# Performance work log

Measured on AMD Instinct MI355X. Metric: run time of the kernel, lower is better.

Reference implementation:

```python
import jax, jax.numpy as jnp
import numpy as np

N_EMBD = 768
N_HEAD = 12

def setup_inputs() -> dict:
    key = jax.random.key(0)
    k_x, k_wa, k_ba, k_wp, k_bp = jax.random.split(key, 5)
    C = N_EMBD
    scale = 1.0 / np.sqrt(C)
    return {
        "x": jax.random.normal(k_x, (2, 4096, C), dtype=jnp.float32),
        "W_attn": jax.random.normal(k_wa, (C, 3 * C), dtype=jnp.float32) * scale,
        "b_attn": jax.random.normal(k_ba, (3 * C,), dtype=jnp.float32) * 0.01,
        "W_proj": jax.random.normal(k_wp, (C, C), dtype=jnp.float32) * scale,
        "b_proj": jax.random.normal(k_bp, (C,), dtype=jnp.float32) * 0.01,
    }

def reference(x, W_attn, b_attn, W_proj, b_proj) -> jnp.ndarray:
    B, T, C = x.shape
    H = N_HEAD
    D = C // H  # head dim
    qkv = x @ W_attn + b_attn                     # [B,T,3C]
    q, k, v = jnp.split(qkv, 3, axis=-1)
    # [B,T,C] -> [B,H,T,D]
    q = q.reshape(B, T, H, D).transpose(0, 2, 1, 3)
    k = k.reshape(B, T, H, D).transpose(0, 2, 1, 3)
    v = v.reshape(B, T, H, D).transpose(0, 2, 1, 3)
    scores = jnp.einsum("bhqd,bhkd->bhqk", q, k) * (1.0 / jnp.sqrt(jnp.float32(D)))
    attn = jax.nn.softmax(scores, axis=-1)        # dropout p=0.0 -> identity
    y = jnp.einsum("bhqk,bhkd->bhqd", attn, v)    # [B,H,T,D]
    y = y.transpose(0, 2, 1, 3).reshape(B, T, C)
    return y @ W_proj + b_proj
```

## Files before the change

kernel.cpp:

```cpp
#include <hip/hip_runtime.h>
#include <stdint.h>

#define NB 2
#define NT 4096
#define NC 768
#define NH 12
#define ND 64
#define NBT (NB*NT)
#define NQKV (3*NC)

typedef _Float16 half_t;
typedef __attribute__((ext_vector_type(8))) _Float16 f16x8;
typedef __attribute__((ext_vector_type(4))) _Float16 f16x4;
typedef __attribute__((ext_vector_type(2))) __fp16 fp16x2;
typedef __attribute__((ext_vector_type(4))) float f32x4;

#define MFMA16(a,b,c) __builtin_amdgcn_mfma_f32_16x16x32_f16((a),(b),(c),0,0,0)

__device__ __forceinline__ void load_lds16(const void* g, void* l) {
    auto gp = reinterpret_cast<__attribute__((address_space(1))) char*>(reinterpret_cast<uintptr_t>(g));
    auto lp = reinterpret_cast<__attribute__((address_space(3))) char*>(reinterpret_cast<uintptr_t>(l));
    __builtin_amdgcn_global_load_lds(gp, lp, 16, 0, 0);
}

__global__ __launch_bounds__(256) void k_pack(const float* __restrict__ in, half_t* __restrict__ out, int n4) {
    int i = blockIdx.x * 256 + threadIdx.x;
    if (i >= n4) return;
    float4 f = reinterpret_cast<const float4*>(in)[i];
    f16x4 h;
    h[0] = (half_t)f.x; h[1] = (half_t)f.y; h[2] = (half_t)f.z; h[3] = (half_t)f.w;
    reinterpret_cast<f16x4*>(out)[i] = h;
}

__global__ __launch_bounds__(256) void k_packT(const float* __restrict__ in, half_t* __restrict__ out, int N, int K) {
    int idx = blockIdx.x * 256 + threadIdx.x;
    if (idx >= N * K) return;
    int n = idx / K, k = idx - n * K;
    out[idx] = (half_t)in[(size_t)k * N + n];
}

template<int OUTF32>
__global__ __launch_bounds__(256) void k_gemm(const half_t* __restrict__ A, const half_t* __restrict__ Bt,
                                              const float* __restrict__ bias, void* __restrict__ out, int N) {
    __shared__ half_t As[128 * 32];
    __shared__ half_t Bs[128 * 32];
    const int tid = threadIdx.x;
    const int lane = tid & 63, w = tid >> 6;
    const int m0 = blockIdx.x * 128, n0 = blockIdx.y * 128;
    const int wm = (w >> 1) * 64, wn = (w & 1) * 64;
    const int lr = lane & 15, lk = (lane >> 4) * 8;

    f32x4 acc[4][4];
#pragma unroll
    for (int a = 0; a < 4; ++a)
#pragma unroll
        for (int bq = 0; bq < 4; ++bq) acc[a][bq] = (f32x4){0.f, 0.f, 0.f, 0.f};

    const int c0 = tid, c1 = 256 + tid;
    const int ldsbase = (tid & ~63) * 16;

    for (int ks = 0; ks < 24; ++ks) {
        const int k0 = ks * 32;
        __syncthreads();
        load_lds16(A  + (size_t)(m0 + (c0 >> 2)) * NC + k0 + (c0 & 3) * 8, (char*)As + ldsbase);
        load_lds16(Bt + (size_t)(n0 + (c0 >> 2)) * NC + k0 + (c0 & 3) * 8, (char*)Bs + ldsbase);
        load_lds16(A  + (size_t)(m0 + (c1 >> 2)) * NC + k0 + (c1 & 3) * 8, (char*)As + 4096 + ldsbase);
        load_lds16(Bt + (size_t)(n0 + (c1 >> 2)) * NC + k0 + (c1 & 3) * 8, (char*)Bs + 4096 + ldsbase);
        __syncthreads();
        f16x8 af[4], bf[4];
#pragma unroll
        for (int mi = 0; mi < 4; ++mi)
            af[mi] = *reinterpret_cast<const f16x8*>(&As[(wm + mi * 16 + lr) * 32 + lk]);
#pragma unroll
        for (int ni = 0; ni < 4; ++ni)
            bf[ni] = *reinterpret_cast<const f16x8*>(&Bs[(wn + ni * 16 + lr) * 32 + lk]);
#pragma unroll
        for (int mi = 0; mi < 4; ++mi)
#pragma unroll
            for (int ni = 0; ni < 4; ++ni)
                acc[mi][ni] = MFMA16(af[mi], bf[ni], acc[mi][ni]);
    }

    const int rg = (lane >> 4) * 4;
#pragma unroll
    for (int ni = 0; ni < 4; ++ni) {
        const int gn = n0 + wn + ni * 16 + lr;
        const float bv = bias[gn];
#pragma unroll
        for (int mi = 0; mi < 4; ++mi)
#pragma unroll
            for (int i = 0; i < 4; ++i) {
                const size_t gm = (size_t)(m0 + wm + mi * 16 + rg + i);
                const float v = acc[mi][ni][i] + bv;
                if (OUTF32) reinterpret_cast<float*>(out)[gm * N + gn] = v;
                else        reinterpret_cast<half_t*>(out)[gm * N + gn] = (half_t)v;
            }
    }
}

__global__ __launch_bounds__(256) void k_vt(const half_t* __restrict__ qkv, half_t* __restrict__ Vt) {
    __shared__ half_t tile[64][72];
    const int tid = threadIdx.x;
    const int t0 = blockIdx.x * 64, bh = blockIdx.y;
    const int b = bh / NH, h = bh - b * NH;
    {
        const int tl = tid >> 2, dc = (tid & 3) * 16;
        const half_t* src = qkv + (size_t)(b * NT + t0 + tl) * NQKV + 2 * NC + h * ND + dc;
        f16x8 v0 = *reinterpret_cast<const f16x8*>(src);
        f16x8 v1 = *reinterpret_cast<const f16x8*>(src + 8);
        *reinterpret_cast<f16x8*>(&tile[tl][dc]) = v0;
        *reinterpret_cast<f16x8*>(&tile[tl][dc + 8]) = v1;
    }
    __syncthreads();
    {
        const int d = tid >> 2, tc = (tid & 3) * 16;
        half_t* dst = Vt + ((size_t)bh * ND + d) * NT + t0 + tc;
        f16x8 o0, o1;
#pragma unroll
        for (int j = 0; j < 8; ++j) o0[j] = tile[tc + j][d];
#pragma unroll
        for (int j = 0; j < 8; ++j) o1[j] = tile[tc + 8 + j][d];
        *reinterpret_cast<f16x8*>(dst) = o0;
        *reinterpret_cast<f16x8*>(dst + 8) = o1;
    }
}

__global__ __launch_bounds__(256, 3) void k_attn(const half_t* __restrict__ qkv, const half_t* __restrict__ Vt,
                                                 half_t* __restrict__ Y) {
    __shared__ half_t Kb[3][64 * 64];
    __shared__ half_t Vb[3][64 * 64];
    const int tid = threadIdx.x, lane = tid & 63, w = tid >> 6;
    const int lr = lane & 15, g = lane >> 4;
    const int qt = blockIdx.x, bh = blockIdx.y;
    const int b = bh / NH, h = bh - b * NH;
    const half_t* Qp = qkv + (size_t)b * NT * NQKV + h * ND;
    const half_t* Kp = Qp + NC;
    const half_t* Vbase = Vt + (size_t)bh * ND * NT;
    const int q0 = qt * 128 + w * 32;

    const int sr = tid >> 3;
    const int colh = (((tid & 7) << 3)) ^ ((sr & 7) << 3);
    const int wub = (tid & ~63) * 16;

    f16x8 aq[2][2];
    const half_t cch = (half_t)(0.125f * 1.4426950408889634f);
#pragma unroll
    for (int qf = 0; qf < 2; ++qf)
#pragma unroll
        for (int dh = 0; dh < 2; ++dh) {
            aq[qf][dh] = *reinterpret_cast<const f16x8*>(&Qp[(size_t)(q0 + qf * 16 + lr) * NQKV + dh * 32 + g * 8]);
#pragma unroll
            for (int j = 0; j < 8; ++j) aq[qf][dh][j] = aq[qf][dh][j] * cch;
        }

    const int swk = (lr & 7) << 3;
    const int cA = (g * 8) ^ swk;
    const int cB = (32 + g * 8) ^ swk;
    const int psw = lr & 7;
    const int goff = (g & 1) << 2;
    const int vc[2][2] = { { (((g >> 1) + 0) ^ psw) * 8 + goff, (((g >> 1) + 2) ^ psw) * 8 + goff },
                           { (((g >> 1) + 4) ^ psw) * 8 + goff, (((g >> 1) + 6) ^ psw) * 8 + goff } };

    f32x4 y[2][4];
#pragma unroll
    for (int qf = 0; qf < 2; ++qf)
#pragma unroll
        for (int df = 0; df < 4; ++df) y[qf][df] = (f32x4){0.f, 0.f, 0.f, 0.f};
    float l_[2] = {0.f, 0.f};

    auto stagebuf = [&](int buf, const half_t* Ks, const half_t* Vs) {
        char* kdst = (char*)&Kb[buf][0] + wub;
        char* vdst = (char*)&Vb[buf][0] + wub;
        load_lds16(Ks, kdst);
        load_lds16(Ks + (size_t)32 * NQKV, kdst + 4096);
        load_lds16(Vs, vdst);
        load_lds16(Vs + (size_t)32 * NT, vdst + 4096);
    };

    const half_t* ksrc = Kp + (size_t)sr * NQKV + colh;
    const half_t* vsrc = Vbase + (size_t)sr * NT + colh;
    stagebuf(0, ksrc, vsrc);
    stagebuf(1, ksrc + (size_t)64 * NQKV, vsrc + 64);
    ksrc += (size_t)128 * NQKV;
    vsrc += 128;

    asm volatile("s_waitcnt vmcnt(4)" ::: "memory");
    __builtin_amdgcn_sched_barrier(0);
    __builtin_amdgcn_s_barrier();
    __builtin_amdgcn_sched_barrier(0);

    int cur = 0, nxt = 2;

    for (int t = 0; t < NT / 64; ++t) {
        if (t + 2 < NT / 64) {
            stagebuf(nxt, ksrc, vsrc);
            ksrc += (size_t)64 * NQKV;
            vsrc += 64;
            nxt = (nxt == 2) ? 0 : nxt + 1;
        }

        f32x4 s[2][4];
#pragma unroll
        for (int st = 0; st < 4; ++st) { s[0][st] = (f32x4){0.f,0.f,0.f,0.f}; s[1][st] = (f32x4){0.f,0.f,0.f,0.f}; }
        const half_t* Kc = &Kb[cur][0];
        __builtin_amdgcn_s_setprio(1);
#pragma unroll
        for (int st = 0; st < 4; ++st) {
            f16x8 bk0 = *reinterpret_cast<const f16x8*>(&Kc[(st * 16 + lr) * 64 + cA]);
            s[0][st] = MFMA16(bk0, aq[0][0], s[0][st]);
            s[1][st] = MFMA16(bk0, aq[1][0], s[1][st]);
            f16x8 bk1 = *reinterpret_cast<const f16x8*>(&Kc[(st * 16 + lr) * 64 + cB]);
            s[0][st] = MFMA16(bk1, aq[0][1], s[0][st]);
            s[1][st] = MFMA16(bk1, aq[1][1], s[1][st]);
        }
        __builtin_amdgcn_s_setprio(0);

        f16x8 pb[2][2];
#pragma unroll
        for (int qf = 0; qf < 2; ++qf) {
            float ps = 0.f;
#pragma unroll
            for (int ks = 0; ks < 2; ++ks) {
                union { f16x8 v; fp16x2 h[4]; } u;
#pragma unroll
                for (int hs = 0; hs < 2; ++hs) {
                    const int st = 2 * ks + hs;
                    const float p0 = __builtin_amdgcn_exp2f(s[qf][st][0]);
                    const float p1 = __builtin_amdgcn_exp2f(s[qf][st][1]);
                    const float p2 = __builtin_amdgcn_exp2f(s[qf][st][2]);
                    const float p3 = __builtin_amdgcn_exp2f(s[qf][st][3]);
                    u.h[2 * hs]     = __builtin_amdgcn_cvt_pkrtz(p0, p1);
                    u.h[2 * hs + 1] = __builtin_amdgcn_cvt_pkrtz(p2, p3);
                    ps += (p0 + p1) + (p2 + p3);
                }
                pb[qf][ks] = u.v;
            }
            l_[qf] += ps;
        }

        const half_t* Vc = &Vb[cur][0];
        __builtin_amdgcn_s_setprio(1);
#pragma unroll
        for (int ks = 0; ks < 2; ++ks)
#pragma unroll
            for (int df = 0; df < 4; ++df) {
                const half_t* vrow = &Vc[(df * 16 + lr) * 64];
                union { f16x8 v; f16x4 q[2]; } va;
                va.q[0] = *reinterpret_cast<const f16x4*>(vrow + vc[ks][0]);
                va.q[1] = *reinterpret_cast<const f16x4*>(vrow + vc[ks][1]);
                y[0][df] = MFMA16(va.v, pb[0][ks], y[0][df]);
                y[1][df] = MFMA16(va.v, pb[1][ks], y[1][df]);
            }
        __builtin_amdgcn_s_setprio(0);

        if (t < NT / 64 - 1) {
            if (t + 2 < NT / 64) { asm volatile("s_waitcnt vmcnt(4)" ::: "memory"); }
            else                 { asm volatile("s_waitcnt vmcnt(0)" ::: "memory"); }
            __builtin_amdgcn_sched_barrier(0);
            __builtin_amdgcn_s_barrier();
            __builtin_amdgcn_sched_barrier(0);
        }
        cur = (cur == 2) ? 0 : cur + 1;
    }

#pragma unroll
    for (int qf = 0; qf < 2; ++qf) {
        float l = l_[qf];
        l += __shfl_xor(l, 16);
        l += __shfl_xor(l, 32);
        const float rl = 1.f / l;
        half_t* Yp = Y + (size_t)(b * NT + q0 + qf * 16 + lr) * NC + h * ND + g * 4;
#pragma unroll
        for (int df = 0; df < 4; ++df) {
            union { f16x4 v; fp16x2 hh[2]; } o;
            o.hh[0] = __builtin_amdgcn_cvt_pkrtz(y[qf][df][0] * rl, y[qf][df][1] * rl);
            o.hh[1] = __builtin_amdgcn_cvt_pkrtz(y[qf][df][2] * rl, y[qf][df][3] * rl);
            *reinterpret_cast<f16x4*>(Yp + df * 16) = o.v;
        }
    }
}

extern "C" void kernel_launch(void* const* d_in, const int* in_sizes, int n_in,
                              void* d_out, int out_size, void* d_ws, size_t ws_size,
                              hipStream_t stream) {
    const float* x  = (const float*)d_in[0];
    const float* Wa = (const float*)d_in[1];
    const float* ba = (const float*)d_in[2];
    const float* Wp = (const float*)d_in[3];
    const float* bp = (const float*)d_in[4];
    float* out = (float*)d_out;

    char* ws = (char*)d_ws;
    half_t* xh   = (half_t*)ws; ws += (size_t)NBT * NC * 2;
    half_t* Wat  = (half_t*)ws; ws += (size_t)NQKV * NC * 2;
    half_t* Wpt  = (half_t*)ws; ws += (size_t)NC * NC * 2;
    half_t* qkvh = (half_t*)ws; ws += (size_t)NBT * NQKV * 2;
    half_t* vt   = (half_t*)ws; ws += (size_t)NB * NH * ND * NT * 2;
    half_t* yh   = (half_t*)ws; ws += (size_t)NBT * NC * 2;

    k_pack<<<(NBT * NC / 4 + 255) / 256, 256, 0, stream>>>(x, xh, NBT * NC / 4);
    k_packT<<<(NQKV * NC + 255) / 256, 256, 0, stream>>>(Wa, Wat, NQKV, NC);
    k_packT<<<(NC * NC + 255) / 256, 256, 0, stream>>>(Wp, Wpt, NC, NC);
    k_gemm<0><<<dim3(NBT / 128, NQKV / 128), 256, 0, stream>>>(xh, Wat, ba, qkvh, NQKV);
    k_vt<<<dim3(NT / 64, NB * NH), 256, 0, stream>>>(qkvh, vt);
    k_attn<<<dim3(NT / 128, NB * NH), 256, 0, stream>>>(qkvh, vt, yh);
    k_gemm<1><<<dim3(NBT / 128, NC / 128), 256, 0, stream>>>(yh, Wpt, bp, out, NC);
}
```

Measured before the change: 216.5 us.

## Software-pipeline QK^T of next KV block with softmax and PV of current

```diff
diff --git a/kernel.cpp b/kernel.cpp
--- a/kernel.cpp
+++ b/kernel.cpp
@@ -125,6 +125,85 @@
     }
 }
 
+#define QKT_BLK(SN)                                                              \
+    {                                                                            \
+        const half_t* Kc = &Kb[kb][0];                                           \
+        _Pragma("unroll")                                                        \
+        for (int st = 0; st < 4; ++st) {                                         \
+            SN[0][st] = (f32x4){0.f, 0.f, 0.f, 0.f};                             \
+            SN[1][st] = (f32x4){0.f, 0.f, 0.f, 0.f};                             \
+        }                                                                        \
+        __builtin_amdgcn_s_setprio(1);                                           \
+        _Pragma("unroll")                                                        \
+        for (int st = 0; st < 4; ++st) {                                         \
+            f16x8 bk0 = *reinterpret_cast<const f16x8*>(&Kc[(st * 16 + lr) * 64 + cA]); \
+            SN[0][st] = MFMA16(bk0, aq[0][0], SN[0][st]);                        \
+            SN[1][st] = MFMA16(bk0, aq[1][0], SN[1][st]);                        \
+            f16x8 bk1 = *reinterpret_cast<const f16x8*>(&Kc[(st * 16 + lr) * 64 + cB]); \
+            SN[0][st] = MFMA16(bk1, aq[0][1], SN[0][st]);                        \
+            SN[1][st] = MFMA16(bk1, aq[1][1], SN[1][st]);                        \
+        }                                                                        \
+        __builtin_amdgcn_s_setprio(0);                                           \
+        kb = (kb == 2) ? 0 : kb + 1;                                             \
+    }
+
+#define SMAX_PV_BLK(SC)                                                          \
+    {                                                                            \
+        f16x8 pb[2][2];                                                          \
+        _Pragma("unroll")                                                        \
+        for (int qf = 0; qf < 2; ++qf) {                                         \
+            float ps = 0.f;                                                      \
+            _Pragma("unroll")                                                    \
+            for (int ks = 0; ks < 2; ++ks) {                                     \
+                union { f16x8 v; fp16x2 h[4]; } u;                               \
+                _Pragma("unroll")                                                \
+                for (int hs = 0; hs < 2; ++hs) {                                 \
+                    const int st = 2 * ks + hs;                                  \
+                    const float p0 = __builtin_amdgcn_exp2f(SC[qf][st][0]);      \
+                    const float p1 = __builtin_amdgcn_exp2f(SC[qf][st][1]);      \
+                    const float p2 = __builtin_amdgcn_exp2f(SC[qf][st][2]);      \
+                    const float p3 = __builtin_amdgcn_exp2f(SC[qf][st][3]);      \
+                    u.h[2 * hs]     = __builtin_amdgcn_cvt_pkrtz(p0, p1);        \
+                    u.h[2 * hs + 1] = __builtin_amdgcn_cvt_pkrtz(p2, p3);        \
+                    ps += (p0 + p1) + (p2 + p3);                                 \
+                }                                                                \
+                pb[qf][ks] = u.v;                                                \
+            }                                                                    \
+            l_[qf] += ps;                                                        \
+        }                                                                        \
+        const half_t* Vc = &Vb[vb][0];                                           \
+        __builtin_amdgcn_s_setprio(1);                                           \
+        _Pragma("unroll")                                                        \
+        for (int ks = 0; ks < 2; ++ks)                                           \
+            _Pragma("unroll")                                                    \
+            for (int df = 0; df < 4; ++df) {                                     \
+                const half_t* vrow = &Vc[(df * 16 + lr) * 64];                   \
+                union { f16x8 v; f16x4 q[2]; } va;                               \
+                va.q[0] = *reinterpret_cast<const f16x4*>(vrow + vc[ks][0]);     \
+                va.q[1] = *reinterpret_cast<const f16x4*>(vrow + vc[ks][1]);     \
+                y[0][df] = MFMA16(va.v, pb[0][ks], y[0][df]);                    \
+                y[1][df] = MFMA16(va.v, pb[1][ks], y[1][df]);                    \
+            }                                                                    \
+        __builtin_amdgcn_s_setprio(0);                                           \
+        vb = (vb == 2) ? 0 : vb + 1;                                             \
+    }
+
+#define STAGE_ADV()                                                              \
+    {                                                                            \
+        stagebuf(sb, ksrc, vsrc);                                                \
+        ksrc += (size_t)64 * NQKV;                                               \
+        vsrc += 64;                                                              \
+        sb = (sb == 2) ? 0 : sb + 1;                                             \
+    }
+
+#define BARRIER_N(N)                                                             \
+    {                                                                            \
+        asm volatile("s_waitcnt vmcnt(" #N ")" ::: "memory");                    \
+        __builtin_amdgcn_sched_barrier(0);                                       \
+        __builtin_amdgcn_s_barrier();                                            \
+        __builtin_amdgcn_sched_barrier(0);                                       \
+    }
+
 __global__ __launch_bounds__(256, 3) void k_attn(const half_t* __restrict__ qkv, const half_t* __restrict__ Vt,
                                                  half_t* __restrict__ Y) {
     __shared__ half_t Kb[3][64 * 64];
@@ -184,84 +263,27 @@
     ksrc += (size_t)128 * NQKV;
     vsrc += 128;
 
-    asm volatile("s_waitcnt vmcnt(4)" ::: "memory");
-    __builtin_amdgcn_sched_barrier(0);
-    __builtin_amdgcn_s_barrier();
-    __builtin_amdgcn_sched_barrier(0);
-
-    int cur = 0, nxt = 2;
-
-    for (int t = 0; t < NT / 64; ++t) {
-        if (t + 2 < NT / 64) {
-            stagebuf(nxt, ksrc, vsrc);
-            ksrc += (size_t)64 * NQKV;
-            vsrc += 64;
-            nxt = (nxt == 2) ? 0 : nxt + 1;
-        }
-
-        f32x4 s[2][4];
-#pragma unroll
-        for (int st = 0; st < 4; ++st) { s[0][st] = (f32x4){0.f,0.f,0.f,0.f}; s[1][st] = (f32x4){0.f,0.f,0.f,0.f}; }
-        const half_t* Kc = &Kb[cur][0];
-        __builtin_amdgcn_s_setprio(1);
-#pragma unroll
-        for (int st = 0; st < 4; ++st) {
-            f16x8 bk0 = *reinterpret_cast<const f16x8*>(&Kc[(st * 16 + lr) * 64 + cA]);
-            s[0][st] = MFMA16(bk0, aq[0][0], s[0][st]);
-            s[1][st] = MFMA16(bk0, aq[1][0], s[1][st]);
-            f16x8 bk1 = *reinterpret_cast<const f16x8*>(&Kc[(st * 16 + lr) * 64 + cB]);
-            s[0][st] = MFMA16(bk1, aq[0][1], s[0][st]);
-            s[1][st] = MFMA16(bk1, aq[1][1], s[1][st]);
-        }
-        __builtin_amdgcn_s_setprio(0);
-
-        f16x8 pb[2][2];
-#pragma unroll
-        for (int qf = 0; qf < 2; ++qf) {
-            float ps = 0.f;
-#pragma unroll
-            for (int ks = 0; ks < 2; ++ks) {
-                union { f16x8 v; fp16x2 h[4]; } u;
-#pragma unroll
-                for (int hs = 0; hs < 2; ++hs) {
-                    const int st = 2 * ks + hs;
-                    const float p0 = __builtin_amdgcn_exp2f(s[qf][st][0]);
-                    const float p1 = __builtin_amdgcn_exp2f(s[qf][st][1]);
-                    const float p2 = __builtin_amdgcn_exp2f(s[qf][st][2]);
-                    const float p3 = __builtin_amdgcn_exp2f(s[qf][st][3]);
-                    u.h[2 * hs]     = __builtin_amdgcn_cvt_pkrtz(p0, p1);
-                    u.h[2 * hs + 1] = __builtin_amdgcn_cvt_pkrtz(p2, p3);
-                    ps += (p0 + p1) + (p2 + p3);
-                }
-                pb[qf][ks] = u.v;
-            }
-            l_[qf] += ps;
-        }
-
-        const half_t* Vc = &Vb[cur][0];
-        __builtin_amdgcn_s_setprio(1);
-#pragma unroll
-        for (int ks = 0; ks < 2; ++ks)
-#pragma unroll
-            for (int df = 0; df < 4; ++df) {
-                const half_t* vrow = &Vc[(df * 16 + lr) * 64];
-                union { f16x8 v; f16x4 q[2]; } va;
-                va.q[0] = *reinterpret_cast<const f16x4*>(vrow + vc[ks][0]);
-                va.q[1] = *reinterpret_cast<const f16x4*>(vrow + vc[ks][1]);
-                y[0][df] = MFMA16(va.v, pb[0][ks], y[0][df]);
-                y[1][df] = MFMA16(va.v, pb[1][ks], y[1][df]);
-            }
-        __builtin_amdgcn_s_setprio(0);
-
-        if (t < NT / 64 - 1) {
-            if (t + 2 < NT / 64) { asm volatile("s_waitcnt vmcnt(4)" ::: "memory"); }
-            else                 { asm volatile("s_waitcnt vmcnt(0)" ::: "memory"); }
-            __builtin_amdgcn_sched_barrier(0);
-            __builtin_amdgcn_s_barrier();
-            __builtin_amdgcn_sched_barrier(0);
-        }
-        cur = (cur == 2) ? 0 : cur + 1;
-    }
+    BARRIER_N(2)
+
+    f32x4 sA[2][4], sB[2][4];
+    int kb = 0, vb = 0, sb = 2;
+
+    QKT_BLK(sA)
+
+    for (int t2 = 0; t2 < 31; ++t2) {
+        STAGE_ADV()
+        QKT_BLK(sB)
+        SMAX_PV_BLK(sA)
+        BARRIER_N(2)
+        STAGE_ADV()
+        QKT_BLK(sA)
+        SMAX_PV_BLK(sB)
+        BARRIER_N(2)
+    }
+    QKT_BLK(sB)
+    SMAX_PV_BLK(sA)
+    BARRIER_N(0)
+    SMAX_PV_BLK(sB)
 
 #pragma unroll
     for (int qf = 0; qf < 2; ++qf) {
```

Result: slower. 675.1 us (+211.8%).
